# Performance work log

Measured on AMD Instinct MI355X. Metric: run time of the kernel, lower is better.

Reference implementation:

```python
import jax, jax.numpy as jnp
import numpy as np

N_KERNELS = 11

def _kernel_mus(n):
    l = [1.0]
    bs = 2.0 / (n - 1)
    l.append(1 - bs / 2)
    for i in range(1, n - 1):
        l.append(l[i] - bs)
    return l

def _kernel_sigmas(n):
    bs = 2.0 / (n - 1)
    return [0.001] + [0.5 * bs] * (n - 1)

MU = jnp.asarray(_kernel_mus(N_KERNELS), jnp.float32)      # [K]
SIGMA = jnp.asarray(_kernel_sigmas(N_KERNELS), jnp.float32)  # [K]


def setup_inputs() -> dict:
    key = jax.random.key(0)
    ks = jax.random.split(key, 10)
    V, E, C = 50000, 300, 128
    B, Q, D = 128, 30, 200
    inp = {
        'query_tokens': jax.random.randint(ks[0], (B, Q), 0, V),
        'document_tokens': jax.random.randint(ks[1], (B, D), 0, V),
        'embedding': jax.random.normal(ks[2], (V, E), jnp.float32) * 0.1,
        'conv_w1': jax.random.normal(ks[3], (C, E, 1), jnp.float32) * 0.05,
        'conv_w2': jax.random.normal(ks[4], (C, E, 2), jnp.float32) * 0.05,
        'conv_w3': jax.random.normal(ks[5], (C, E, 3), jnp.float32) * 0.05,
        'conv_b1': jax.random.normal(ks[6], (C,), jnp.float32) * 0.01,
        'conv_b2': jax.random.normal(ks[7], (C,), jnp.float32) * 0.01,
        'conv_b3': jax.random.normal(ks[8], (C,), jnp.float32) * 0.01,
        'dense_w': jax.random.uniform(ks[9], (1, N_KERNELS * 9), jnp.float32, -0.014, 0.014),
    }
    return inp


def _conv_ngram(x_ble, w, b):
    # x_ble: [B, L, E]; w: [C, E, k]; pad (0, k-1) on the length dim -> same length out
    x = x_ble.transpose(0, 2, 1)  # [B, E, L]
    y = jax.lax.conv_general_dilated(
        x, w, window_strides=(1,), padding=[(0, w.shape[2] - 1)],
        dimension_numbers=('NCH', 'OIH', 'NCH'))
    return jax.nn.relu(y + b[None, :, None]).transpose(0, 2, 1)  # [B, L, C]


def _kernel_pool(q, d, qd_mask, q_mask):
    # q: [B,Q,C], d: [B,D,C]; cosine sim -> Gaussian RBF soft-binning -> masked log-sum pooling
    qn = q / (jnp.linalg.norm(q, axis=-1, keepdims=True) + 1e-13)
    dn = d / (jnp.linalg.norm(d, axis=-1, keepdims=True) + 1e-13)
    cos = jnp.einsum('bqc,bdc->bqd', qn, dn) * qd_mask           # [B,Q,D]
    diff = cos[..., None] - MU                                    # [B,Q,D,K]
    kern = jnp.exp(-(diff * diff) / (2.0 * SIGMA * SIGMA)) * qd_mask[..., None]
    per_kernel_query = jnp.sum(kern, axis=2)                      # [B,Q,K]
    logk = jnp.log(jnp.clip(per_kernel_query, 1e-10)) * 0.01
    return jnp.sum(logk * q_mask[..., None], axis=1)              # [B,K]


def reference(query_tokens, document_tokens, embedding,
              conv_w1, conv_w2, conv_w3, conv_b1, conv_b2, conv_b3, dense_w):
    q_mask = (query_tokens > 0).astype(jnp.float32)               # [B,Q]
    d_mask = (document_tokens > 0).astype(jnp.float32)            # [B,D]
    qd_mask = q_mask[:, :, None] * d_mask[:, None, :]             # [B,Q,D]

    q_emb = embedding[query_tokens]                               # [B,Q,E]
    d_emb = embedding[document_tokens]                            # [B,D,E]

    convs = [(conv_w1, conv_b1), (conv_w2, conv_b2), (conv_w3, conv_b3)]
    q_grams = [_conv_ngram(q_emb, w, b) for w, b in convs]
    d_grams = [_conv_ngram(d_emb, w, b) for w, b in convs]

    feats = jnp.concatenate(
        [_kernel_pool(q, d, qd_mask, q_mask) for q in q_grams for d in d_grams],
        axis=1)                                                   # [B, K*9]
    return (feats @ dense_w.T)[:, 0]                              # [B]
```

## Files before the change

kernel.cpp:

```cpp
#include <hip/hip_runtime.h>
#include <hip/hip_bf16.h>
#include <math.h>

#define B_   128
#define Qn   30
#define Dn   200
#define En   300

typedef __attribute__((ext_vector_type(8))) short short8;
typedef __attribute__((ext_vector_type(4))) float floatx4;
typedef unsigned int u32;
typedef unsigned short u16;

static __device__ __forceinline__ u16 f2b(float x) {
    union { float f; u32 u; } v; v.f = x;
    u32 r = v.u + 0x7FFFu + ((v.u >> 16) & 1u);
    return (u16)(r >> 16);
}
static __device__ __forceinline__ float bits2f(u32 u) {
    union { u32 u2; float f; } v; v.u2 = u; return v.f;
}

__global__ void prep_kernel(
    const float* __restrict__ w1, const float* __restrict__ w2, const float* __restrict__ w3,
    u16* __restrict__ Wt3)
{
    int p = (blockIdx.x*128 + blockIdx.y)*256 + threadIdx.x;
    if (p >= 245760) return;
    int ks = p / 24576;
    int r  = p - ks*24576;
    int g, rr;
    if (r < 4096)        { g = 0; rr = r;         }
    else if (r < 12288)  { g = 1; rr = r - 4096;  }
    else                 { g = 2; rr = r - 12288; }
    int j  = rr >> 12;
    int r2 = rr & 4095;
    int nt  = r2 >> 9;
    int q4  = (r2 >> 7) & 3;
    int c16 = (r2 >> 3) & 15;
    int k8  = r2 & 7;
    int ch = nt*16 + c16;
    int e  = ks*32 + q4*8 + k8;
    float v = 0.f;
    if (e < En) {
        if (g == 0)      v = w1[ch*En + e];
        else if (g == 1) v = w2[(ch*En + e)*2 + j];
        else             v = w3[(ch*En + e)*3 + j];
    }
    Wt3[p] = f2b(v);
}

__global__ __launch_bounds__(512, 4) void conv_kernel(
    const int* __restrict__ qtok, const int* __restrict__ dtok,
    const float* __restrict__ emb,
    const u16* __restrict__ Wt3,
    const float* __restrict__ b1, const float* __restrict__ b2, const float* __restrict__ b3,
    u16* __restrict__ qg, u16* __restrict__ dg,
    float* __restrict__ invnq, float* __restrict__ invnd)
{
    __shared__ __align__(16) char smem[43560];
    char* As  = smem;
    int*  toks = (int*)(smem + 43296);

    const int tile = blockIdx.x;
    const int tid = threadIdx.x;
    const int wv = tid >> 6, lane = tid & 63;
    const int l15 = lane & 15, qd4 = lane >> 4;
    const int mh = wv >> 2, nh = wv & 3;
    const int gR0 = tile*64;

    if (tid < 66) {
        int gr = gR0 + tid;
        int t = -1;
        if (gr < 32768) {
            int b = gr >> 8, pos = gr & 255;
            if (pos < Dn) t = dtok[b*Dn + pos];
            else if (pos >= 208 && pos < 238) t = qtok[b*Qn + (pos - 208)];
        }
        toks[tid] = t;
    }
    __syncthreads();

    #pragma unroll
    for (int i = 0; i < 6; ++i) {
        int idx = tid + i*512;
        if (idx < 2640) {
            int r = idx / 40, c4 = idx - r*40;
            int t = toks[r];
            u16 o0=0,o1=0,o2=0,o3=0;
            if (t >= 0) {
                float4 v = *(const float4*)(emb + t*En + c4*4);
                o0=f2b(v.x); o1=f2b(v.y); o2=f2b(v.z); o3=f2b(v.w);
            }
            u16* pdst = (u16*)(As + r*656 + c4*8);
            pdst[0]=o0; pdst[1]=o1; pdst[2]=o2; pdst[3]=o3;
        }
    }

    float bias[3][2];
    #pragma unroll
    for (int nt = 0; nt < 2; ++nt) {
        int ch = nh*32 + nt*16 + l15;
        bias[0][nt] = b1[ch];
        bias[1][nt] = b2[ch];
        bias[2][nt] = b3[ch];
    }

    floatx4 acc[3][2][2];
    #pragma unroll
    for (int g = 0; g < 3; ++g)
        #pragma unroll
        for (int mt = 0; mt < 2; ++mt)
            #pragma unroll
            for (int nt = 0; nt < 2; ++nt)
                acc[g][mt][nt] = (floatx4){0.f,0.f,0.f,0.f};

    __syncthreads();

    float4 hf[6];
    #pragma unroll
    for (int i = 0; i < 6; ++i) {
        int idx = tid + i*512;
        const float* p = emb;
        if (idx < 2640) {
            int r = idx / 40, c = idx - r*40;
            int t = toks[r];
            if (t >= 0 && c < 35) p = emb + t*En + (40 + c)*4;
        }
        hf[i] = *(const float4*)p;
    }

    #pragma unroll 1
    for (int ks = 0; ks < 5; ++ks) {
        short8 af[2][3];
        #pragma unroll
        for (int mt = 0; mt < 2; ++mt)
            #pragma unroll
            for (int j = 0; j < 3; ++j)
                af[mt][j] = *(const short8*)(As + (mh*32 + mt*16 + l15 + j)*656 + ks*64 + qd4*16);
        const u16* Wks = Wt3 + ks*24576;
        #pragma unroll
        for (int g = 0; g < 3; ++g) {
            const int cbW = (g == 0) ? 0 : (g == 1) ? 4096 : 12288;
            #pragma unroll
            for (int j = 0; j <= g; ++j) {
                const u16* bb = Wks + cbW + (j*8 + nh*2)*512 + lane*8;
                short8 w0  = *(const short8*)(bb);
                short8 w1v = *(const short8*)(bb + 512);
                #pragma unroll
                for (int mt = 0; mt < 2; ++mt) {
                    acc[g][mt][0] = __builtin_amdgcn_mfma_f32_16x16x32_bf16(
                        af[mt][j], w0,  acc[g][mt][0], 0, 0, 0);
                    acc[g][mt][1] = __builtin_amdgcn_mfma_f32_16x16x32_bf16(
                        af[mt][j], w1v, acc[g][mt][1], 0, 0, 0);
                }
            }
        }
    }

    #pragma unroll
    for (int i = 0; i < 6; ++i) {
        int idx = tid + i*512;
        if (idx < 2640) {
            int r = idx / 40, c = idx - r*40;
            int t = toks[r];
            bool ok = (t >= 0) && (c < 35);
            u16 o0=0,o1=0,o2=0,o3=0;
            if (ok) { o0=f2b(hf[i].x); o1=f2b(hf[i].y); o2=f2b(hf[i].z); o3=f2b(hf[i].w); }
            u16* pdst = (u16*)(As + r*656 + (40 + c)*8);
            pdst[0]=o0; pdst[1]=o1; pdst[2]=o2; pdst[3]=o3;
        }
    }
    __syncthreads();

    #pragma unroll 1
    for (int ks = 5; ks < 10; ++ks) {
        short8 af[2][3];
        #pragma unroll
        for (int mt = 0; mt < 2; ++mt)
            #pragma unroll
            for (int j = 0; j < 3; ++j)
                af[mt][j] = *(const short8*)(As + (mh*32 + mt*16 + l15 + j)*656 + ks*64 + qd4*16);
        const u16* Wks = Wt3 + ks*24576;
        #pragma unroll
        for (int g = 0; g < 3; ++g) {
            const int cbW = (g == 0) ? 0 : (g == 1) ? 4096 : 12288;
            #pragma unroll
            for (int j = 0; j <= g; ++j) {
                const u16* bb = Wks + cbW + (j*8 + nh*2)*512 + lane*8;
                short8 w0  = *(const short8*)(bb);
                short8 w1v = *(const short8*)(bb + 512);
                #pragma unroll
                for (int mt = 0; mt < 2; ++mt) {
                    acc[g][mt][0] = __builtin_amdgcn_mfma_f32_16x16x32_bf16(
                        af[mt][j], w0,  acc[g][mt][0], 0, 0, 0);
                    acc[g][mt][1] = __builtin_amdgcn_mfma_f32_16x16x32_bf16(
                        af[mt][j], w1v, acc[g][mt][1], 0, 0, 0);
                }
            }
        }
    }

    u16* Gs = (u16*)smem;
    #pragma unroll
    for (int g = 0; g < 3; ++g) {
        __syncthreads();
        #pragma unroll
        for (int mt = 0; mt < 2; ++mt)
            #pragma unroll
            for (int nt = 0; nt < 2; ++nt) {
                int ch = nh*32 + nt*16 + l15;
                #pragma unroll
                for (int i = 0; i < 4; ++i) {
                    int row = mh*32 + mt*16 + qd4*4 + i;
                    Gs[row*136 + ch] = f2b(fmaxf(acc[g][mt][nt][i] + bias[g][nt], 0.f));
                }
            }
        __syncthreads();

        {
            int r = tid >> 3, pp = tid & 7;
            const char* rp = (const char*)Gs + r*272 + pp*32;
            float ssum = 0.f;
            #pragma unroll
            for (int t2 = 0; t2 < 2; ++t2) {
                uint4 u = *(const uint4*)(rp + t2*16);
                float x;
                x = bits2f(u.x << 16); ssum += x*x;  x = bits2f(u.x & 0xffff0000u); ssum += x*x;
                x = bits2f(u.y << 16); ssum += x*x;  x = bits2f(u.y & 0xffff0000u); ssum += x*x;
                x = bits2f(u.z << 16); ssum += x*x;  x = bits2f(u.z & 0xffff0000u); ssum += x*x;
                x = bits2f(u.w << 16); ssum += x*x;  x = bits2f(u.w & 0xffff0000u); ssum += x*x;
            }
            ssum += __shfl_xor(ssum, 1);
            ssum += __shfl_xor(ssum, 2);
            ssum += __shfl_xor(ssum, 4);
            if (pp == 0) {
                float inv = 1.f / (sqrtf(ssum) + 1e-13f);
                int gr = gR0 + r;
                int b = gr >> 8, pos = gr & 255;
                if (pos < 208)      invnd[(g*B_ + b)*208 + pos] = inv;
                else if (pos < 238) invnq[(g*B_ + b)*32 + (pos - 208)] = inv;
            }
        }
        #pragma unroll
        for (int i = 0; i < 2; ++i) {
            int idx = tid + i*512;
            int r = idx >> 4, c16 = idx & 15;
            uint4 v = *(const uint4*)((const char*)Gs + r*272 + c16*16);
            int gr = gR0 + r;
            int b = gr >> 8, pos = gr & 255;
            if (pos < 208)      *(uint4*)(dg + ((g*B_ + b)*208 + pos)*128 + c16*8) = v;
            else if (pos < 238) *(uint4*)(qg + ((g*B_ + b)*32 + (pos - 208))*128 + c16*8) = v;
        }
    }
}

__global__ __launch_bounds__(512, 4) void pool_kernel(
    const u16* __restrict__ qg, const u16* __restrict__ dg,
    const float* __restrict__ invnq, const float* __restrict__ invnd,
    const int* __restrict__ qtok, const int* __restrict__ dtok,
    float* __restrict__ feats)
{
    __shared__ __align__(16) u16 dsb[208*136];
    __shared__ float pk[96*12];
    __shared__ float invqA[96];
    __shared__ float qmA[96];
    __shared__ __align__(16) float invd[208];

    const int tid = threadIdx.x;
    const int b = blockIdx.y, dj = blockIdx.x;
    const int wv = tid >> 6, lane = tid & 63;
    const int l15 = lane & 15, qd4 = lane >> 4;

    for (int idx = tid; idx < 208*16; idx += 512) {
        int r = idx >> 4, ch = idx & 15;
        uint4 v = make_uint4(0u,0u,0u,0u);
        if (r < Dn) v = *(const uint4*)(dg + ((dj*B_ + b)*208 + r)*128 + ch*8);
        *(uint4*)((char*)dsb + r*272 + ch*16) = v;
    }
    if (tid < 208) {
        float v = invnd[(dj*B_ + b)*208 + tid];
        bool ok = (tid < Dn) && (dtok[b*Dn + tid] > 0);
        invd[tid] = ok ? v : (-fabsf(v) - 1.0f);
    }
    if (tid < 96) {
        int qi = tid >> 5, qr = tid & 31;
        float v = invnq[(qi*B_ + b)*32 + qr];
        bool ok = (qr < Qn) && (qtok[b*Qn + qr] > 0);
        invqA[tid] = ok ? v : 0.f;
        qmA[tid] = ok ? 1.f : 0.f;
    }
    for (int i = tid; i < 96*12; i += 512) pk[i] = 0.f;
    __syncthreads();

    const float CkR[9] = {8886110.5f, 162754.79f, 2980.958f, 54.598150f, 1.0f,
                          0.018315639f, 3.3546263e-4f, 6.1442124e-6f, 1.1253517e-7f};

    for (int qi = 0; qi < 3; ++qi) {
        short8 qf[2][4];
        float vq[2];
        #pragma unroll
        for (int qt = 0; qt < 2; ++qt) {
            vq[qt] = invqA[qi*32 + qt*16 + l15];
            #pragma unroll
            for (int ks = 0; ks < 4; ++ks)
                qf[qt][ks] = *(const short8*)(qg + ((qi*B_ + b)*32 + qt*16 + l15)*128 + ks*32 + qd4*8);
        }
        float pkl[2][11];
        #pragma unroll
        for (int qt = 0; qt < 2; ++qt)
            #pragma unroll
            for (int k = 0; k < 11; ++k) pkl[qt][k] = 0.f;

        for (int t = wv; t < 13; t += 8) {
            short8 af[4];
            #pragma unroll
            for (int ks = 0; ks < 4; ++ks)
                af[ks] = *(const short8*)((const char*)dsb + (t*16 + l15)*272 + ks*64 + qd4*16);
            floatx4 acc[2];
            acc[0] = (floatx4){0.f,0.f,0.f,0.f};
            acc[1] = (floatx4){0.f,0.f,0.f,0.f};
            #pragma unroll
            for (int ks = 0; ks < 4; ++ks)
                #pragma unroll
                for (int qt = 0; qt < 2; ++qt)
                    acc[qt] = __builtin_amdgcn_mfma_f32_16x16x32_bf16(af[ks], qf[qt][ks], acc[qt], 0, 0, 0);
            floatx4 iv4 = *(const floatx4*)(invd + t*16 + qd4*4);
            #pragma unroll
            for (int qt = 0; qt < 2; ++qt)
                #pragma unroll
                for (int i = 0; i < 4; ++i) {
                    float cs = acc[qt][i] * vq[qt] * iv4[i];
                    cs = (cs > 0.f) ? cs : 2.0f;
                    float t0 = cs - 1.0f;
                    float u  = cs - 0.9f;
                    float s0 = __expf(-500000.f * t0 * t0);
                    float e  = __expf(-50.f * u * u);
                    float rr = __expf(-20.f * cs);
                    pkl[qt][0] += s0;
                    pkl[qt][1] += e;
                    #pragma unroll
                    for (int kk = 0; kk < 9; ++kk) {
                        e = e * rr * CkR[kk];
                        pkl[qt][2 + kk] += e;
                    }
                }
        }
        #pragma unroll
        for (int qt = 0; qt < 2; ++qt)
            #pragma unroll
            for (int k = 0; k < 11; ++k) {
                float v = pkl[qt][k];
                v += __shfl_xor(v, 16);
                v += __shfl_xor(v, 32);
                if (qd4 == 0) atomicAdd(&pk[(qi*32 + qt*16 + l15)*12 + k], v);
            }
    }
    __syncthreads();

    if (tid < 264) {
        int qik = tid >> 3, qc = tid & 7;
        int qi = qik / 11, k = qik - qi*11;
        float s = 0.f;
        #pragma unroll
        for (int i = 0; i < 4; ++i) {
            int q = qc*4 + i;
            s += qmA[qi*32 + q] * 0.01f * __logf(fmaxf(pk[(qi*32 + q)*12 + k], 1e-10f));
        }
        s += __shfl_xor(s, 1);
        s += __shfl_xor(s, 2);
        s += __shfl_xor(s, 4);
        if (qc == 0) feats[(b*9 + qi*3 + dj)*11 + k] = s;
    }
}

__global__ void final_kernel(const float* __restrict__ feats,
                             const float* __restrict__ dw,
                             float* __restrict__ out) {
    int b = threadIdx.x;
    if (b < B_) {
        float s = 0.f;
        for (int f = 0; f < 99; ++f) s += feats[b*99 + f] * dw[f];
        out[b] = s;
    }
}

extern "C" void kernel_launch(void* const* d_in, const int* in_sizes, int n_in,
                              void* d_out, int out_size, void* d_ws, size_t ws_size,
                              hipStream_t stream) {
    const int*   qtok = (const int*)d_in[0];
    const int*   dtok = (const int*)d_in[1];
    const float* emb  = (const float*)d_in[2];
    const float* w1   = (const float*)d_in[3];
    const float* w2   = (const float*)d_in[4];
    const float* w3   = (const float*)d_in[5];
    const float* b1   = (const float*)d_in[6];
    const float* b2   = (const float*)d_in[7];
    const float* b3   = (const float*)d_in[8];
    const float* dw   = (const float*)d_in[9];
    float* out = (float*)d_out;

    char* w = (char*)d_ws;
    u16*   Wt3   = (u16*)w;
    u16*   qg    = (u16*)(w + 491520);
    u16*   dgm   = (u16*)(w + 3637248);
    float* invq_ = (float*)(w + 24084480);
    float* invd_ = (float*)(w + 24133632);
    float* feats = (float*)(w + 24453120);

    prep_kernel<<<dim3(8, B_), 256, 0, stream>>>(w1, w2, w3, Wt3);

    conv_kernel<<<dim3(512), 512, 0, stream>>>(
        qtok, dtok, emb, Wt3, b1, b2, b3, qg, dgm, invq_, invd_);

    pool_kernel<<<dim3(3, B_), 512, 0, stream>>>(qg, dgm, invq_, invd_, qtok, dtok, feats);

    final_kernel<<<1, 128, 0, stream>>>(feats, dw, out);
}
```

Before: 175.2 us.

## Split pool kernel over document tiles with global atomic accumulation

The pool kernel now splits the 13 document tiles across 4 blocks along a new grid z dimension, using 256 threads per block instead of 512 with each wave handling at most one tile. Per-query kernel sums are atomically added into a global buffer, which prep_kernel zeroes in extra blocks. The log/mask pooling and dense dot product move into a per-batch final kernel. This gives more and smaller blocks for better CU occupancy and load balance, at the cost of global atomics and an extra pass over the partial sums.

```diff
diff --git a/kernel.cpp b/kernel.cpp
--- a/kernel.cpp
+++ b/kernel.cpp
@@ -23,8 +23,15 @@
 
 __global__ void prep_kernel(
     const float* __restrict__ w1, const float* __restrict__ w2, const float* __restrict__ w3,
-    u16* __restrict__ Wt3)
+    u16* __restrict__ Wt3, float* __restrict__ pkg)
 {
+    if (blockIdx.x >= 8) {
+        int zi = ((blockIdx.x - 8)*128 + blockIdx.y)*256 + threadIdx.x;
+        if (zi < 442368) pkg[zi] = 0.f;
+        int zi2 = zi + 229376;
+        if (zi2 < 442368) pkg[zi2] = 0.f;
+        return;
+    }
     int p = (blockIdx.x*128 + blockIdx.y)*256 + threadIdx.x;
     if (p >= 245760) return;
     int ks = p / 24576;
@@ -255,32 +262,37 @@
     }
 }
 
-__global__ __launch_bounds__(512, 4) void pool_kernel(
+__global__ __launch_bounds__(256, 2) void pool_kernel(
     const u16* __restrict__ qg, const u16* __restrict__ dg,
     const float* __restrict__ invnq, const float* __restrict__ invnd,
     const int* __restrict__ qtok, const int* __restrict__ dtok,
-    float* __restrict__ feats)
+    float* __restrict__ pkg)
 {
-    __shared__ __align__(16) u16 dsb[208*136];
+    __shared__ __align__(16) u16 dsb[64*136];
     __shared__ float pk[96*12];
     __shared__ float invqA[96];
-    __shared__ float qmA[96];
-    __shared__ __align__(16) float invd[208];
+    __shared__ __align__(16) float invd[64];
 
     const int tid = threadIdx.x;
-    const int b = blockIdx.y, dj = blockIdx.x;
+    const int b = blockIdx.y, dj = blockIdx.x, th = blockIdx.z;
     const int wv = tid >> 6, lane = tid & 63;
     const int l15 = lane & 15, qd4 = lane >> 4;
 
-    for (int idx = tid; idx < 208*16; idx += 512) {
+    const int ts = (th == 0) ? 0 : (th == 1) ? 4 : (th == 2) ? 7 : 10;
+    const int te = (th == 0) ? 4 : (th == 1) ? 7 : (th == 2) ? 10 : 13;
+    const int r0 = ts*16, nrows = (te - ts)*16;
+
+    for (int idx = tid; idx < nrows*16; idx += 256) {
         int r = idx >> 4, ch = idx & 15;
+        int gr = r0 + r;
         uint4 v = make_uint4(0u,0u,0u,0u);
-        if (r < Dn) v = *(const uint4*)(dg + ((dj*B_ + b)*208 + r)*128 + ch*8);
+        if (gr < Dn) v = *(const uint4*)(dg + ((dj*B_ + b)*208 + gr)*128 + ch*8);
         *(uint4*)((char*)dsb + r*272 + ch*16) = v;
     }
-    if (tid < 208) {
-        float v = invnd[(dj*B_ + b)*208 + tid];
-        bool ok = (tid < Dn) && (dtok[b*Dn + tid] > 0);
+    if (tid < nrows) {
+        int gr = r0 + tid;
+        float v = invnd[(dj*B_ + b)*208 + gr];
+        bool ok = (gr < Dn) && (dtok[b*Dn + gr] > 0);
         invd[tid] = ok ? v : (-fabsf(v) - 1.0f);
     }
     if (tid < 96) {
@@ -288,13 +300,16 @@
         float v = invnq[(qi*B_ + b)*32 + qr];
         bool ok = (qr < Qn) && (qtok[b*Qn + qr] > 0);
         invqA[tid] = ok ? v : 0.f;
-        qmA[tid] = ok ? 1.f : 0.f;
-    }
-    for (int i = tid; i < 96*12; i += 512) pk[i] = 0.f;
+    }
+    for (int i = tid; i < 96*12; i += 256) pk[i] = 0.f;
     __syncthreads();
 
     const float CkR[9] = {8886110.5f, 162754.79f, 2980.958f, 54.598150f, 1.0f,
                           0.018315639f, 3.3546263e-4f, 6.1442124e-6f, 1.1253517e-7f};
+
+    const int t = ts + wv;
+    const bool active = (t < te);
+    const int tl = t - ts;
 
     for (int qi = 0; qi < 3; ++qi) {
         short8 qf[2][4];
@@ -312,11 +327,11 @@
             #pragma unroll
             for (int k = 0; k < 11; ++k) pkl[qt][k] = 0.f;
 
-        for (int t = wv; t < 13; t += 8) {
+        if (active) {
             short8 af[4];
             #pragma unroll
             for (int ks = 0; ks < 4; ++ks)
-                af[ks] = *(const short8*)((const char*)dsb + (t*16 + l15)*272 + ks*64 + qd4*16);
+                af[ks] = *(const short8*)((const char*)dsb + (tl*16 + l15)*272 + ks*64 + qd4*16);
             floatx4 acc[2];
             acc[0] = (floatx4){0.f,0.f,0.f,0.f};
             acc[1] = (floatx4){0.f,0.f,0.f,0.f};
@@ -325,7 +340,7 @@
                 #pragma unroll
                 for (int qt = 0; qt < 2; ++qt)
                     acc[qt] = __builtin_amdgcn_mfma_f32_16x16x32_bf16(af[ks], qf[qt][ks], acc[qt], 0, 0, 0);
-            floatx4 iv4 = *(const floatx4*)(invd + t*16 + qd4*4);
+            floatx4 iv4 = *(const floatx4*)(invd + tl*16 + qd4*4);
             #pragma unroll
             for (int qt = 0; qt < 2; ++qt)
                 #pragma unroll
@@ -345,44 +360,74 @@
                         pkl[qt][2 + kk] += e;
                     }
                 }
-        }
-        #pragma unroll
-        for (int qt = 0; qt < 2; ++qt)
-            #pragma unroll
-            for (int k = 0; k < 11; ++k) {
-                float v = pkl[qt][k];
-                v += __shfl_xor(v, 16);
-                v += __shfl_xor(v, 32);
-                if (qd4 == 0) atomicAdd(&pk[(qi*32 + qt*16 + l15)*12 + k], v);
-            }
-    }
-    __syncthreads();
-
-    if (tid < 264) {
-        int qik = tid >> 3, qc = tid & 7;
-        int qi = qik / 11, k = qik - qi*11;
-        float s = 0.f;
-        #pragma unroll
-        for (int i = 0; i < 4; ++i) {
-            int q = qc*4 + i;
-            s += qmA[qi*32 + q] * 0.01f * __logf(fmaxf(pk[(qi*32 + q)*12 + k], 1e-10f));
-        }
-        s += __shfl_xor(s, 1);
-        s += __shfl_xor(s, 2);
-        s += __shfl_xor(s, 4);
-        if (qc == 0) feats[(b*9 + qi*3 + dj)*11 + k] = s;
-    }
-}
-
-__global__ void final_kernel(const float* __restrict__ feats,
-                             const float* __restrict__ dw,
-                             float* __restrict__ out) {
-    int b = threadIdx.x;
-    if (b < B_) {
-        float s = 0.f;
-        for (int f = 0; f < 99; ++f) s += feats[b*99 + f] * dw[f];
-        out[b] = s;
-    }
+            #pragma unroll
+            for (int qt = 0; qt < 2; ++qt)
+                #pragma unroll
+                for (int k = 0; k < 11; ++k) {
+                    float v = pkl[qt][k];
+                    v += __shfl_xor(v, 16);
+                    v += __shfl_xor(v, 32);
+                    if (qd4 == 0) atomicAdd(&pk[(qi*32 + qt*16 + l15)*12 + k], v);
+                }
+        }
+    }
+    __syncthreads();
+
+    float* dst = pkg + (b*3 + dj)*1152;
+    #pragma unroll
+    for (int i = 0; i < 5; ++i) {
+        int idx = tid + i*256;
+        if (idx < 1152) atomicAdd(&dst[idx], pk[idx]);
+    }
+}
+
+__global__ __launch_bounds__(256, 2) void final_kernel(
+    const float* __restrict__ pkg, const int* __restrict__ qtok,
+    const float* __restrict__ dw, float* __restrict__ out)
+{
+    __shared__ float qm[96];
+    __shared__ float fl[99];
+    __shared__ float red[256];
+
+    const int tid = threadIdx.x;
+    const int b = blockIdx.x;
+
+    if (tid < 96) {
+        int qr = tid & 31;
+        qm[tid] = ((qr < Qn) && (qtok[b*Qn + qr] > 0)) ? 1.f : 0.f;
+    }
+    __syncthreads();
+
+    #pragma unroll
+    for (int s = 0; s < 4; ++s) {
+        int slot = tid + s*256;
+        if (slot < 792) {
+            int pair = slot >> 3, qc = slot & 7;
+            int dji = pair / 11, k = pair - dji*11;
+            int qi = dji / 3, dj = dji - qi*3;
+            const float* pp = pkg + (b*3 + dj)*1152;
+            float ps = 0.f;
+            #pragma unroll
+            for (int i = 0; i < 4; ++i) {
+                int q = qc*4 + i;
+                ps += qm[qi*32 + q] * 0.01f * __logf(fmaxf(pp[(qi*32 + q)*12 + k], 1e-10f));
+            }
+            ps += __shfl_xor(ps, 1);
+            ps += __shfl_xor(ps, 2);
+            ps += __shfl_xor(ps, 4);
+            if (qc == 0) fl[pair] = ps;
+        }
+    }
+    __syncthreads();
+
+    red[tid] = (tid < 99) ? fl[tid] * dw[tid] : 0.f;
+    __syncthreads();
+    #pragma unroll
+    for (int s = 128; s > 0; s >>= 1) {
+        if (tid < s) red[tid] += red[tid + s];
+        __syncthreads();
+    }
+    if (tid == 0) out[b] = red[0];
 }
 
 extern "C" void kernel_launch(void* const* d_in, const int* in_sizes, int n_in,
@@ -406,14 +451,14 @@
     u16*   dgm   = (u16*)(w + 3637248);
     float* invq_ = (float*)(w + 24084480);
     float* invd_ = (float*)(w + 24133632);
-    float* feats = (float*)(w + 24453120);
-
-    prep_kernel<<<dim3(8, B_), 256, 0, stream>>>(w1, w2, w3, Wt3);
+    float* pkg   = (float*)(w + 24453120);
+
+    prep_kernel<<<dim3(15, B_), 256, 0, stream>>>(w1, w2, w3, Wt3, pkg);
 
     conv_kernel<<<dim3(512), 512, 0, stream>>>(
         qtok, dtok, emb, Wt3, b1, b2, b3, qg, dgm, invq_, invd_);
 
-    pool_kernel<<<dim3(3, B_), 512, 0, stream>>>(qg, dgm, invq_, invd_, qtok, dtok, feats);
-
-    final_kernel<<<1, 128, 0, stream>>>(feats, dw, out);
-}
+    pool_kernel<<<dim3(3, B_, 4), 256, 0, stream>>>(qg, dgm, invq_, invd_, qtok, dtok, pkg);
+
+    final_kernel<<<B_, 256, 0, stream>>>(pkg, qtok, dw, out);
+}
```

New measurement: 181.0 us. +3.3%, slower.
